# Performance work log

Measured on AMD Instinct MI355X. Metric: run time of the kernel, lower is better.

## Reference

```python
import jax, jax.numpy as jnp
import numpy as np

DEPTH, DIM, HEADS = 12, 768, 12
B, N = 2, 2048
HEAD_DIM = DIM // HEADS


def setup_inputs() -> dict:
    key = jax.random.key(0)
    ks = jax.random.split(key, 8)
    s = 0.02
    return {
        "x": jax.random.normal(ks[0], (B, N, DIM), jnp.float32),
        "sequence_ids": jnp.sort(jax.random.randint(ks[1], (B, N), 0, 8), axis=-1),
        "sequence_mask": jnp.zeros((B, N), dtype=bool),
        "ln1_w": jnp.ones((DEPTH, DIM), jnp.float32),
        "ln1_b": jnp.zeros((DEPTH, DIM), jnp.float32),
        "qkv_w": jax.random.normal(ks[2], (DEPTH, DIM, 3 * DIM), jnp.float32) * s,
        "qkv_b": jnp.zeros((DEPTH, 3 * DIM), jnp.float32),
        "proj_w": jax.random.normal(ks[3], (DEPTH, DIM, DIM), jnp.float32) * s,
        "proj_b": jnp.zeros((DEPTH, DIM), jnp.float32),
        "ls1_g": jnp.full((DEPTH, DIM), 1e-5, jnp.float32),
        "ln2_w": jnp.ones((DEPTH, DIM), jnp.float32),
        "ln2_b": jnp.zeros((DEPTH, DIM), jnp.float32),
        "fc1_w": jax.random.normal(ks[4], (DEPTH, DIM, 4 * DIM), jnp.float32) * s,
        "fc1_b": jnp.zeros((DEPTH, 4 * DIM), jnp.float32),
        "fc2_w": jax.random.normal(ks[5], (DEPTH, 4 * DIM, DIM), jnp.float32) * s,
        "fc2_b": jnp.zeros((DEPTH, DIM), jnp.float32),
        "ls2_g": jnp.full((DEPTH, DIM), 1e-5, jnp.float32),
        "r": 0,
    }


def _layernorm(x, w, b, eps=1e-5):
    m = x.mean(-1, keepdims=True)
    v = ((x - m) ** 2).mean(-1, keepdims=True)
    return (x - m) * jax.lax.rsqrt(v + eps) * w + b


def _attention(x, attn_mask, qkv_w, qkv_b, proj_w, proj_b):
    b, n, c = x.shape
    qkv = (x @ qkv_w + qkv_b).reshape(b, n, 3, HEADS, HEAD_DIM)
    qkv = jnp.transpose(qkv, (2, 0, 3, 1, 4))  # [3, B, H, N, hd]
    q, k, v = qkv[0], qkv[1], qkv[2]
    attn = jnp.einsum("bhqd,bhkd->bhqk", q, k) * (HEAD_DIM ** -0.5)
    neg_inf = jnp.finfo(attn.dtype).min
    attn = jnp.where(attn_mask[:, None, :, :], neg_inf, attn)  # broadcast over heads
    attn = jax.nn.softmax(attn, axis=-1)
    out = jnp.einsum("bhqk,bhkd->bhqd", attn, v)
    out = jnp.transpose(out, (0, 2, 1, 3)).reshape(b, n, c)
    return out @ proj_w + proj_b


def reference(x, sequence_ids, sequence_mask, ln1_w, ln1_b, qkv_w, qkv_b,
              proj_w, proj_b, ls1_g, ln2_w, ln2_b, fc1_w, fc1_b,
              fc2_w, fc2_b, ls2_g, r):
    # attn_mask: True where attention is NOT allowed
    attn_mask = sequence_ids[:, :, None] != sequence_ids[:, None, :]
    attn_mask = attn_mask | sequence_mask[:, :, None] | sequence_mask[:, None, :]
    for i in range(DEPTH):
        h = _layernorm(x, ln1_w[i], ln1_b[i])
        h = _attention(h, attn_mask, qkv_w[i], qkv_b[i], proj_w[i], proj_b[i])
        x = x + h * ls1_g[i]
        h = _layernorm(x, ln2_w[i], ln2_b[i])
        h = jax.nn.gelu(h @ fc1_w[i] + fc1_b[i], approximate=False) @ fc2_w[i] + fc2_b[i]
        x = x + h * ls2_g[i]
    return x
```

## Files before the change

kernel.cpp:

```cpp
#include <hip/hip_runtime.h>

#define NDEPTH 12
#define NDIM 768
#define NHEADS 12
#define NB 2
#define NSEQ 2048
#define MTOK (NB*NSEQ)

typedef short bf16x8 __attribute__((ext_vector_type(8)));
typedef float f32x4 __attribute__((ext_vector_type(4)));
typedef unsigned short u16;
typedef unsigned int u32;

#define L2E 1.44269504088896f

__device__ inline u16 f2bf(float f){
  union { float f; u32 u; } x; x.f = f;
  u32 r = x.u + 0x7fffu + ((x.u >> 16) & 1u);
  return (u16)(r >> 16);
}

__device__ inline f32x4 mfma16(bf16x8 a, bf16x8 b, f32x4 c){
  return __builtin_amdgcn_mfma_f32_16x16x32_bf16(a, b, c, 0, 0, 0);
}

#define GLOAD_LDS(gsrc, ldst) __builtin_amdgcn_global_load_lds( \
    (const __attribute__((address_space(1))) u32*)(gsrc), \
    (__attribute__((address_space(3))) u32*)(ldst), 16, 0, 0)

__device__ inline void ln_body(const float* __restrict__ x,
    const float* __restrict__ w, const float* __restrict__ b,
    u16* __restrict__ out, int blk){
  int wv = threadIdx.x >> 6, lane = threadIdx.x & 63;
  int row = blk * 4 + wv;
  const float* xr = x + (size_t)row * NDIM;
  float v[12];
  #pragma unroll
  for (int j = 0; j < 12; j++) v[j] = xr[lane + 64*j];
  float s = 0.f;
  #pragma unroll
  for (int j = 0; j < 12; j++) s += v[j];
  #pragma unroll
  for (int m = 1; m < 64; m <<= 1) s += __shfl_xor(s, m);
  float mean = s * (1.0f/768.0f);
  float q = 0.f;
  #pragma unroll
  for (int j = 0; j < 12; j++){ float d = v[j]-mean; q += d*d; }
  #pragma unroll
  for (int m = 1; m < 64; m <<= 1) q += __shfl_xor(q, m);
  float rs = rsqrtf(q * (1.0f/768.0f) + 1e-5f);
  u16* orow = out + (size_t)row * NDIM;
  #pragma unroll
  for (int j = 0; j < 12; j++){
    int c = lane + 64*j;
    orow[c] = f2bf((v[j]-mean)*rs*w[c] + b[c]);
  }
}

__global__ __launch_bounds__(256) void ln_kernel(const float* __restrict__ x,
    const float* __restrict__ w, const float* __restrict__ b,
    u16* __restrict__ out){
  ln_body(x, w, b, out, blockIdx.x);
}

__device__ inline void wtrans_body(const float* __restrict__ in,
    u16* __restrict__ out, int K, int N, int n0, int k0, float* tile){
  int t = threadIdx.x;
  #pragma unroll
  for (int j = 0; j < 16; j++){
    int idx = t + j*256;
    int r = idx >> 6, c = idx & 63;
    tile[r*65 + c] = in[(size_t)(k0+r)*N + n0 + c];
  }
  __syncthreads();
  #pragma unroll
  for (int j = 0; j < 16; j++){
    int idx = t + j*256;
    int c = idx >> 6, r = idx & 63;
    out[(size_t)(n0+c)*K + k0 + r] = f2bf(tile[r*65 + c]);
  }
}

__global__ __launch_bounds__(256) void wtrans_kernel(const float* __restrict__ in,
    u16* __restrict__ out, int K, int N){
  __shared__ float tile[64*65];
  wtrans_body(in, out, K, N, blockIdx.x*64, blockIdx.y*64, tile);
}

__global__ __launch_bounds__(256) void lnwt_kernel(
    const float* __restrict__ x, const float* __restrict__ lw,
    const float* __restrict__ lb, u16* __restrict__ lout,
    const float* __restrict__ qkvw, const float* __restrict__ projw,
    const float* __restrict__ fc1w, const float* __restrict__ fc2w,
    u16* __restrict__ wq, u16* __restrict__ wp,
    u16* __restrict__ w1, u16* __restrict__ w2){
  __shared__ float tile[64*65];
  int bid = blockIdx.x;
  if (bid < 1024){ ln_body(x, lw, lb, lout, bid); return; }
  bid -= 1024;
  const float* in; u16* out; int K, N, tl;
  if (bid < 432){        in = qkvw; out = wq; K = 768;  N = 2304; tl = bid; }
  else if (bid < 576){   in = projw; out = wp; K = 768; N = 768;  tl = bid - 432; }
  else if (bid < 1152){  in = fc1w; out = w1; K = 768;  N = 3072; tl = bid - 576; }
  else {                 in = fc2w; out = w2; K = 3072; N = 768;  tl = bid - 1152; }
  int ntn = N >> 6;
  int n0 = (tl % ntn) << 6, k0 = (tl / ntn) << 6;
  wtrans_body(in, out, K, N, n0, k0, tile);
}

template<int BN, int EPI>
__global__ __launch_bounds__(512) void gemm_kernel(
    const u16* __restrict__ A, const u16* __restrict__ Wt,
    const float* __restrict__ bias, const float* __restrict__ g,
    u16* __restrict__ outb, float* __restrict__ xres,
    int M, int N, int K)
{
  constexpr int WGN = BN / 32;
  constexpr int WGM = 8 / WGN;
  constexpr int WTM = 128 / WGM;
  constexpr int MI = WTM / 16;
  constexpr int NI = 2;
  __shared__ u16 As[2][128*64];
  __shared__ u16 Bs[2][BN*64];
  int nwg = gridDim.x;
  int bid = (blockIdx.x & 7) * (nwg >> 3) + (blockIdx.x >> 3);
  int nt = N / BN;
  int bm = bid / nt, bn = bid % nt;
  int m0 = bm*128, n0 = bn*BN;
  int t = threadIdx.x, lane = t & 63, wv = t >> 6;
  int wm = (wv / WGN) * WTM, wn = (wv % WGN) * 32;
  f32x4 acc[MI][NI] = {};
  int fr = lane & 15, fg = lane >> 4;

  auto stage = [&](int bf, int k0){
    #pragma unroll
    for (int i = 0; i < 2; i++){
      int off = t*16 + i*8192;
      int row = off >> 7, cb = off & 127;
      const char* src = (const char*)A + ((size_t)(m0+row)*K + k0)*2 + (cb ^ ((row&7)<<4));
      GLOAD_LDS(src, (char*)As[bf] + off);
    }
    #pragma unroll
    for (int i = 0; i < BN/64; i++){
      int off = t*16 + i*8192;
      int row = off >> 7, cb = off & 127;
      const char* src = (const char*)Wt + ((size_t)(n0+row)*K + k0)*2 + (cb ^ ((row&7)<<4));
      GLOAD_LDS(src, (char*)Bs[bf] + off);
    }
  };

  stage(0, 0);
  int cur = 0;
  for (int k0 = 0; k0 < K; k0 += 64){
    __syncthreads();
    if (k0 + 64 < K) stage(cur ^ 1, k0 + 64);

    bf16x8 af[MI][2], bfv[NI][2];
    #pragma unroll
    for (int mi = 0; mi < MI; mi++)
      #pragma unroll
      for (int kh = 0; kh < 2; kh++){
        int row = wm + mi*16 + fr;
        int off = (row*128 + kh*64 + fg*16) ^ ((row&7)<<4);
        af[mi][kh] = *(const bf16x8*)((const char*)As[cur] + off);
      }
    #pragma unroll
    for (int ni = 0; ni < NI; ni++)
      #pragma unroll
      for (int kh = 0; kh < 2; kh++){
        int row = wn + ni*16 + fr;
        int off = (row*128 + kh*64 + fg*16) ^ ((row&7)<<4);
        bfv[ni][kh] = *(const bf16x8*)((const char*)Bs[cur] + off);
      }
    #pragma unroll
    for (int mi = 0; mi < MI; mi++)
      #pragma unroll
      for (int ni = 0; ni < NI; ni++){
        acc[mi][ni] = mfma16(af[mi][0], bfv[ni][0], acc[mi][ni]);
        acc[mi][ni] = mfma16(af[mi][1], bfv[ni][1], acc[mi][ni]);
      }
    cur ^= 1;
  }

  int fq = fg << 2;
  #pragma unroll
  for (int mi = 0; mi < MI; mi++){
    #pragma unroll
    for (int ni = 0; ni < NI; ni++){
      int col = n0 + wn + ni*16 + fr;
      float bv = bias[col];
      #pragma unroll
      for (int r = 0; r < 4; r++){
        int row = m0 + wm + mi*16 + fq + r;
        float v = acc[mi][ni][r] + bv;
        if (EPI == 0){
          outb[(size_t)row * N + col] = f2bf(v);
        } else if (EPI == 1){
          float ge = 0.5f * v * (1.0f + erff(v * 0.70710678118f));
          outb[(size_t)row * N + col] = f2bf(ge);
        } else {
          xres[(size_t)row * N + col] += v * g[col];
        }
      }
    }
  }
}

__global__ __launch_bounds__(256) void attn_kernel(
    const u16* __restrict__ qkv, const int* __restrict__ sid,
    const unsigned char* __restrict__ smask, u16* __restrict__ outb)
{
  __shared__ u16 Ks[64][72];
  __shared__ u16 Vs[64][72];
  __shared__ u16 Ps[4][16][72];
  int nwg = gridDim.x;
  int blk = (blockIdx.x & 7) * (nwg >> 3) + (blockIdx.x >> 3);
  int qt = blk & 31; int bh = blk >> 5;
  int b = bh / NHEADS, h = bh % NHEADS;
  int t = threadIdx.x, lane = t & 63, wv = t >> 6;
  int q0 = qt << 6;
  size_t rowbase = (size_t)b * NSEQ;
  int fr = lane & 15, fg8 = (lane >> 4) << 3, fq = (lane >> 4) << 2;

  int qrow = q0 + (wv << 4) + fr;
  const u16* qp = qkv + (rowbase + qrow) * 2304 + h*64 + fg8;
  bf16x8 qf0 = *(const bf16x8*)qp;
  bf16x8 qf1 = *(const bf16x8*)(qp + 32);

  int qlo = sid[rowbase + q0];
  int qhi = sid[rowbase + q0 + 63];

  int sq[4]; int mq[4];
  #pragma unroll
  for (int r = 0; r < 4; r++){
    int qr = q0 + (wv << 4) + fq + r;
    sq[r] = sid[rowbase + qr];
    mq[r] = smask[rowbase + qr];
  }
  float m[4], l[4]; f32x4 o[4] = {};
  #pragma unroll
  for (int r = 0; r < 4; r++){ m[r] = -3.0e38f; l[r] = 0.f; }

  int skk = t >> 2, sd = (t & 3) << 4;

  for (int kt = 0; kt < NSEQ/64; kt++){
    int klo = sid[rowbase + (kt << 6)];
    int khi = sid[rowbase + (kt << 6) + 63];
    if (khi < qlo || klo > qhi) continue;

    __syncthreads();
    int krow = (kt << 6) + skk;
    const u16* kp = qkv + (rowbase + krow) * 2304 + 768 + h*64 + sd;
    *(uint4*)&Ks[skk][sd]     = *(const uint4*)kp;
    *(uint4*)&Ks[skk][sd + 8] = *(const uint4*)(kp + 8);
    const u16* vp = kp + 768;
    uint4 v0 = *(const uint4*)vp, v1 = *(const uint4*)(vp + 8);
    {
      const u16* vv = (const u16*)&v0;
      #pragma unroll
      for (int i = 0; i < 8; i++) Vs[sd + i][skk] = vv[i];
      vv = (const u16*)&v1;
      #pragma unroll
      for (int i = 0; i < 8; i++) Vs[sd + 8 + i][skk] = vv[i];
    }
    int ks[4]; int mk[4];
    #pragma unroll
    for (int s2 = 0; s2 < 4; s2++){
      int kk = (kt << 6) + (s2 << 4) + fr;
      ks[s2] = sid[rowbase + kk];
      mk[s2] = smask[rowbase + kk];
    }
    __syncthreads();

    f32x4 S[4];
    #pragma unroll
    for (int s2 = 0; s2 < 4; s2++){
      bf16x8 kf0 = *(const bf16x8*)&Ks[(s2 << 4) + fr][fg8];
      bf16x8 kf1 = *(const bf16x8*)&Ks[(s2 << 4) + fr][fg8 + 32];
      f32x4 s = {};
      s = mfma16(qf0, kf0, s);
      s = mfma16(qf1, kf1, s);
      #pragma unroll
      for (int r = 0; r < 4; r++){
        float v = s[r] * 0.125f;
        bool msk = (mq[r] | mk[s2]) || (sq[r] != ks[s2]);
        S[s2][r] = msk ? -3.0e38f : v;
      }
    }
    float mn[4], sf[4], rs[4];
    #pragma unroll
    for (int r = 0; r < 4; r++){
      float mx = fmaxf(fmaxf(S[0][r], S[1][r]), fmaxf(S[2][r], S[3][r]));
      #pragma unroll
      for (int d = 1; d < 16; d <<= 1) mx = fmaxf(mx, __shfl_xor(mx, d));
      mn[r] = fmaxf(m[r], mx);
      sf[r] = exp2f((m[r] - mn[r]) * L2E);
      rs[r] = 0.f;
    }
    #pragma unroll
    for (int s2 = 0; s2 < 4; s2++){
      #pragma unroll
      for (int r = 0; r < 4; r++){
        float p = exp2f((S[s2][r] - mn[r]) * L2E);
        rs[r] += p;
        Ps[wv][fq + r][(s2 << 4) + fr] = f2bf(p);
      }
    }
    #pragma unroll
    for (int r = 0; r < 4; r++){
      #pragma unroll
      for (int d = 1; d < 16; d <<= 1) rs[r] += __shfl_xor(rs[r], d);
      l[r] = l[r] * sf[r] + rs[r];
      m[r] = mn[r];
    }
    #pragma unroll
    for (int dsub = 0; dsub < 4; dsub++)
      #pragma unroll
      for (int r = 0; r < 4; r++) o[dsub][r] *= sf[r];
    __syncthreads();
    #pragma unroll
    for (int kg = 0; kg < 2; kg++){
      bf16x8 pf = *(const bf16x8*)&Ps[wv][fr][(kg << 5) + fg8];
      #pragma unroll
      for (int dsub = 0; dsub < 4; dsub++){
        bf16x8 vf = *(const bf16x8*)&Vs[(dsub << 4) + fr][(kg << 5) + fg8];
        o[dsub] = mfma16(pf, vf, o[dsub]);
      }
    }
  }

  #pragma unroll
  for (int dsub = 0; dsub < 4; dsub++){
    #pragma unroll
    for (int r = 0; r < 4; r++){
      int row = q0 + (wv << 4) + fq + r;
      int col = h*64 + (dsub << 4) + fr;
      outb[(rowbase + row) * NDIM + col] = f2bf(o[dsub][r] / l[r]);
    }
  }
}

extern "C" void kernel_launch(void* const* d_in, const int* in_sizes, int n_in,
                              void* d_out, int out_size, void* d_ws, size_t ws_size,
                              hipStream_t stream) {
  const float* x_in = (const float*)d_in[0];
  const int* sid = (const int*)d_in[1];
  const unsigned char* smask = (const unsigned char*)d_in[2];
  const float* ln1w = (const float*)d_in[3];
  const float* ln1b = (const float*)d_in[4];
  const float* qkvw = (const float*)d_in[5];
  const float* qkvb = (const float*)d_in[6];
  const float* projw = (const float*)d_in[7];
  const float* projb = (const float*)d_in[8];
  const float* ls1 = (const float*)d_in[9];
  const float* ln2w = (const float*)d_in[10];
  const float* ln2b = (const float*)d_in[11];
  const float* fc1w = (const float*)d_in[12];
  const float* fc1b = (const float*)d_in[13];
  const float* fc2w = (const float*)d_in[14];
  const float* fc2b = (const float*)d_in[15];
  const float* ls2 = (const float*)d_in[16];

  float* x = (float*)d_out;
  char* ws = (char*)d_ws;
  u16* hbuf   = (u16*)ws;
  u16* qkvbuf = (u16*)(ws + (size_t)6291456);
  u16* abuf   = (u16*)(ws + (size_t)25165824);
  u16* mbuf   = (u16*)(ws + (size_t)31457280);
  const size_t WT0 = 56623104;

  bool fused_wt = ws_size >= (size_t)(WT0 + 14155776);
  u16* wq; u16* wp; u16* w1; u16* w2;
  if (fused_wt){
    wq = (u16*)(ws + WT0);
    wp = wq + (size_t)2304*768;
    w1 = wp + (size_t)768*768;
    w2 = w1 + (size_t)768*3072;
  } else {
    wq = wp = w1 = w2 = (u16*)(ws + WT0);
  }

  hipMemcpyAsync(x, x_in, (size_t)MTOK*NDIM*4, hipMemcpyDeviceToDevice, stream);

  for (int i = 0; i < NDEPTH; i++){
    const float* qw = qkvw + (size_t)i*NDIM*2304;
    const float* pw = projw + (size_t)i*NDIM*NDIM;
    const float* f1 = fc1w + (size_t)i*NDIM*3072;
    const float* f2 = fc2w + (size_t)i*3072*NDIM;

    if (fused_wt){
      lnwt_kernel<<<2752, 256, 0, stream>>>(x, ln1w + i*NDIM, ln1b + i*NDIM, hbuf,
                                            qw, pw, f1, f2, wq, wp, w1, w2);
    } else {
      ln_kernel<<<MTOK/4, 256, 0, stream>>>(x, ln1w + i*NDIM, ln1b + i*NDIM, hbuf);
      wtrans_kernel<<<dim3(2304/64, 768/64), 256, 0, stream>>>(qw, wq, NDIM, 2304);
    }
    gemm_kernel<128,0><<<(MTOK/128)*(2304/128), 512, 0, stream>>>(
        hbuf, wq, qkvb + (size_t)i*2304, nullptr, qkvbuf, nullptr, MTOK, 2304, NDIM);
    attn_kernel<<<NB*NHEADS*(NSEQ/64), 256, 0, stream>>>(qkvbuf, sid, smask, abuf);
    if (!fused_wt)
      wtrans_kernel<<<dim3(768/64, 768/64), 256, 0, stream>>>(pw, wp, NDIM, NDIM);
    gemm_kernel<64,2><<<(MTOK/128)*(NDIM/64), 512, 0, stream>>>(
        abuf, wp, projb + (size_t)i*NDIM, ls1 + (size_t)i*NDIM,
        nullptr, x, MTOK, NDIM, NDIM);
    ln_kernel<<<MTOK/4, 256, 0, stream>>>(x, ln2w + i*NDIM, ln2b + i*NDIM, hbuf);
    if (!fused_wt)
      wtrans_kernel<<<dim3(3072/64, 768/64), 256, 0, stream>>>(f1, w1, NDIM, 3072);
    gemm_kernel<128,1><<<(MTOK/128)*(3072/128), 512, 0, stream>>>(
        hbuf, w1, fc1b + (size_t)i*3072, nullptr, mbuf, nullptr, MTOK, 3072, NDIM);
    if (!fused_wt)
      wtrans_kernel<<<dim3(768/64, 3072/64), 256, 0, stream>>>(f2, w2, 3072, NDIM);
    gemm_kernel<64,2><<<(MTOK/128)*(NDIM/64), 512, 0, stream>>>(
        mbuf, w2, fc2b + (size_t)i*NDIM, ls2 + (size_t)i*NDIM,
        nullptr, x, MTOK, NDIM, 3072);
  }
}
```

Baseline: 2.079 ms.

## Transpose all layer weights upfront and deepen GEMM global-to-LDS prefetch pipeline

When the workspace is large enough, all twelve layers' weights are converted to transposed bf16 in a single kernel before the layer loop. This replaces the per-layer fused LN plus weight-transpose launch with a plain LN launch. The GEMM main loop now issues loads two k-steps ahead, using explicit vmcnt waits and raw s_barriers instead of a __syncthreads before each stage, so global-to-LDS copies overlap MFMA work more deeply. The cost is a much larger workspace requirement. The smallest-workspace fallback no longer transposes any weights, so that path computes with untransposed weights.

```diff
diff --git a/kernel.cpp b/kernel.cpp
--- a/kernel.cpp
+++ b/kernel.cpp
@@ -79,12 +79,6 @@
     int c = idx >> 6, r = idx & 63;
     out[(size_t)(n0+c)*K + k0 + r] = f2bf(tile[r*65 + c]);
   }
-}
-
-__global__ __launch_bounds__(256) void wtrans_kernel(const float* __restrict__ in,
-    u16* __restrict__ out, int K, int N){
-  __shared__ float tile[64*65];
-  wtrans_body(in, out, K, N, blockIdx.x*64, blockIdx.y*64, tile);
 }
 
 __global__ __launch_bounds__(256) void lnwt_kernel(
@@ -103,6 +97,24 @@
   else if (bid < 576){   in = projw; out = wp; K = 768; N = 768;  tl = bid - 432; }
   else if (bid < 1152){  in = fc1w; out = w1; K = 768;  N = 3072; tl = bid - 576; }
   else {                 in = fc2w; out = w2; K = 3072; N = 768;  tl = bid - 1152; }
+  int ntn = N >> 6;
+  int n0 = (tl % ntn) << 6, k0 = (tl / ntn) << 6;
+  wtrans_body(in, out, K, N, n0, k0, tile);
+}
+
+__global__ __launch_bounds__(256) void wtrans12_kernel(
+    const float* __restrict__ qkvw, const float* __restrict__ projw,
+    const float* __restrict__ fc1w, const float* __restrict__ fc2w,
+    u16* __restrict__ wbase){
+  __shared__ float tile[64*65];
+  int bid = blockIdx.x;
+  int layer = bid / 1728, sub = bid % 1728;
+  u16* wl = wbase + (size_t)layer * 7077888;
+  const float* in; u16* out; int K, N, tl;
+  if (sub < 432){       in = qkvw + (size_t)layer*768*2304; out = wl;                 K = 768;  N = 2304; tl = sub; }
+  else if (sub < 576){  in = projw + (size_t)layer*768*768; out = wl + 1769472;       K = 768;  N = 768;  tl = sub - 432; }
+  else if (sub < 1152){ in = fc1w + (size_t)layer*768*3072; out = wl + 2359296;       K = 768;  N = 3072; tl = sub - 576; }
+  else {                in = fc2w + (size_t)layer*3072*768; out = wl + 4718592;       K = 3072; N = 768;  tl = sub - 1152; }
   int ntn = N >> 6;
   int n0 = (tl % ntn) << 6, k0 = (tl / ntn) << 6;
   wtrans_body(in, out, K, N, n0, k0, tile);
@@ -150,10 +162,13 @@
   };
 
   stage(0, 0);
+  stage(1, 64);
   int cur = 0;
-  for (int k0 = 0; k0 < K; k0 += 64){
-    __syncthreads();
-    if (k0 + 64 < K) stage(cur ^ 1, k0 + 64);
+  int NS = K >> 6;
+  for (int i = 0; i < NS; i++){
+    if constexpr (BN == 128) asm volatile("s_waitcnt vmcnt(4)" ::: "memory");
+    else                     asm volatile("s_waitcnt vmcnt(3)" ::: "memory");
+    asm volatile("s_barrier" ::: "memory");
 
     bf16x8 af[MI][2], bfv[NI][2];
     #pragma unroll
@@ -179,6 +194,9 @@
         acc[mi][ni] = mfma16(af[mi][0], bfv[ni][0], acc[mi][ni]);
         acc[mi][ni] = mfma16(af[mi][1], bfv[ni][1], acc[mi][ni]);
       }
+
+    asm volatile("s_barrier" ::: "memory");
+    if (i + 2 < NS) stage(cur, (i + 2) << 6);
     cur ^= 1;
   }
 
@@ -369,18 +387,14 @@
   u16* mbuf   = (u16*)(ws + (size_t)31457280);
   const size_t WT0 = 56623104;
 
-  bool fused_wt = ws_size >= (size_t)(WT0 + 14155776);
-  u16* wq; u16* wp; u16* w1; u16* w2;
-  if (fused_wt){
-    wq = (u16*)(ws + WT0);
-    wp = wq + (size_t)2304*768;
-    w1 = wp + (size_t)768*768;
-    w2 = w1 + (size_t)768*3072;
-  } else {
-    wq = wp = w1 = w2 = (u16*)(ws + WT0);
-  }
+  bool upfront  = ws_size >= (size_t)226492416;
+  bool fused_wt = !upfront && ws_size >= WT0 + (size_t)14155776;
+  u16* wall = (u16*)(ws + WT0);
 
   hipMemcpyAsync(x, x_in, (size_t)MTOK*NDIM*4, hipMemcpyDeviceToDevice, stream);
+
+  if (upfront)
+    wtrans12_kernel<<<12*1728, 256, 0, stream>>>(qkvw, projw, fc1w, fc2w, wall);
 
   for (int i = 0; i < NDEPTH; i++){
     const float* qw = qkvw + (size_t)i*NDIM*2304;
@@ -388,28 +402,32 @@
     const float* f1 = fc1w + (size_t)i*NDIM*3072;
     const float* f2 = fc2w + (size_t)i*3072*NDIM;
 
+    u16 *wq, *wp, *w1, *w2;
+    if (upfront){
+      wq = wall + (size_t)i*7077888;
+      wp = wq + 1769472; w1 = wp + 589824; w2 = w1 + 2359296;
+    } else if (fused_wt){
+      wq = wall; wp = wq + (size_t)2304*768;
+      w1 = wp + (size_t)768*768; w2 = w1 + (size_t)768*3072;
+    } else {
+      wq = wp = w1 = w2 = wall;
+    }
+
     if (fused_wt){
       lnwt_kernel<<<2752, 256, 0, stream>>>(x, ln1w + i*NDIM, ln1b + i*NDIM, hbuf,
                                             qw, pw, f1, f2, wq, wp, w1, w2);
     } else {
       ln_kernel<<<MTOK/4, 256, 0, stream>>>(x, ln1w + i*NDIM, ln1b + i*NDIM, hbuf);
-      wtrans_kernel<<<dim3(2304/64, 768/64), 256, 0, stream>>>(qw, wq, NDIM, 2304);
     }
     gemm_kernel<128,0><<<(MTOK/128)*(2304/128), 512, 0, stream>>>(
         hbuf, wq, qkvb + (size_t)i*2304, nullptr, qkvbuf, nullptr, MTOK, 2304, NDIM);
     attn_kernel<<<NB*NHEADS*(NSEQ/64), 256, 0, stream>>>(qkvbuf, sid, smask, abuf);
-    if (!fused_wt)
-      wtrans_kernel<<<dim3(768/64, 768/64), 256, 0, stream>>>(pw, wp, NDIM, NDIM);
     gemm_kernel<64,2><<<(MTOK/128)*(NDIM/64), 512, 0, stream>>>(
         abuf, wp, projb + (size_t)i*NDIM, ls1 + (size_t)i*NDIM,
         nullptr, x, MTOK, NDIM, NDIM);
     ln_kernel<<<MTOK/4, 256, 0, stream>>>(x, ln2w + i*NDIM, ln2b + i*NDIM, hbuf);
-    if (!fused_wt)
-      wtrans_kernel<<<dim3(3072/64, 768/64), 256, 0, stream>>>(f1, w1, NDIM, 3072);
     gemm_kernel<128,1><<<(MTOK/128)*(3072/128), 512, 0, stream>>>(
         hbuf, w1, fc1b + (size_t)i*3072, nullptr, mbuf, nullptr, MTOK, 3072, NDIM);
-    if (!fused_wt)
-      wtrans_kernel<<<dim3(768/64, 3072/64), 256, 0, stream>>>(f2, w2, 3072, NDIM);
     gemm_kernel<64,2><<<(MTOK/128)*(NDIM/64), 512, 0, stream>>>(
         mbuf, w2, fc2b + (size_t)i*NDIM, ls2 + (size_t)i*NDIM,
         nullptr, x, MTOK, NDIM, 3072);
```

New measurement: 2.193 ms. +5.5%, slower.
